# Kernel optimization log

Hardware: AMD Instinct MI355X
Metric: run time of the kernel (lower is better)

The kernel has to match this reference:

```python
import jax, jax.numpy as jnp
import numpy as np

DIM = 1024
NUM_HEADS = 16
HEAD_DIM = DIM // NUM_HEADS


def setup_inputs() -> dict:
    key = jax.random.key(0)
    k1, k2, k3 = jax.random.split(key, 3)
    scale = 1.0 / np.sqrt(DIM)
    x = jax.random.normal(k1, (4, 2048, DIM), dtype=jnp.float32)
    w_qkv = jax.random.normal(k2, (DIM, 3 * DIM), dtype=jnp.float32) * scale
    b_qkv = jnp.zeros((3 * DIM,), dtype=jnp.float32)
    w_out = jax.random.normal(k3, (DIM, DIM), dtype=jnp.float32) * scale
    b_out = jnp.zeros((DIM,), dtype=jnp.float32)
    return {"x": x, "w_qkv": w_qkv, "b_qkv": b_qkv, "w_out": w_out, "b_out": b_out}


def reference(x, w_qkv, b_qkv, w_out, b_out):
    B, S, D = x.shape
    H, Hd = NUM_HEADS, HEAD_DIM
    qkv = x @ w_qkv + b_qkv  # [B,S,3D]
    q, k, v = jnp.split(qkv, 3, axis=-1)
    # [B,H,S,Hd]
    q = q.reshape(B, S, H, Hd).transpose(0, 2, 1, 3)
    k = k.reshape(B, S, H, Hd).transpose(0, 2, 1, 3)
    v = v.reshape(B, S, H, Hd).transpose(0, 2, 1, 3)
    scores = jnp.einsum('bhqd,bhkd->bhqk', q, k) / np.sqrt(Hd).astype(np.float32)
    causal = jnp.triu(jnp.ones((S, S), dtype=bool), k=1)  # True above diagonal -> masked
    scores = jnp.where(causal[None, None], -jnp.inf, scores)
    scores = scores - jnp.max(scores, axis=-1, keepdims=True)
    attn = jax.nn.softmax(scores, axis=-1)
    out = jnp.einsum('bhqk,bhkd->bhqd', attn, v)  # [B,H,S,Hd]
    out = out.transpose(0, 2, 1, 3).reshape(B, S, D)
    return out @ w_out + b_out
```

## Files before the change

kernel.cpp:

```cpp
#include <hip/hip_runtime.h>

typedef unsigned short u16;
typedef unsigned int u32;
using f32x4 = __attribute__((ext_vector_type(4))) float;
using u32x4 = __attribute__((ext_vector_type(4))) u32;
typedef u32x4 __attribute__((may_alias)) u32x4a;
typedef uint2 __attribute__((may_alias)) uint2a;
using bf16x8 = __attribute__((ext_vector_type(8))) __bf16;

#define SEQ 2048

__device__ __forceinline__ u16 f2bf(float f) {
  union { float f; u32 u; } c; c.f = f;
  return (u16)((c.u + 0x7fffu + ((c.u >> 16) & 1u)) >> 16);
}
__device__ __forceinline__ float bf2f(u16 h) {
  union { u32 u; float f; } c; c.u = ((u32)h) << 16;
  return c.f;
}
__device__ __forceinline__ bf16x8 ld16(const u16* p) {
  return __builtin_bit_cast(bf16x8, *(const u32x4a*)p);
}
__device__ __forceinline__ f32x4 mfma16(bf16x8 a, bf16x8 b, f32x4 c) {
  return __builtin_amdgcn_mfma_f32_16x16x32_bf16(a, b, c, 0, 0, 0);
}
__device__ __forceinline__ void gload_lds16(const u16* g, u16* l) {
  __builtin_amdgcn_global_load_lds(
      (const __attribute__((address_space(1))) void*)g,
      (__attribute__((address_space(3))) void*)l, 16, 0, 0);
}
__device__ __forceinline__ u32 cvtpk(float lo, float hi) {
  u32 r;
  asm("v_cvt_pk_bf16_f32 %0, %1, %2" : "=v"(r) : "v"(lo), "v"(hi));
  return r;
}
__device__ __forceinline__ void plane32_swap(u32& a, u32& b) {
  asm("v_permlane32_swap_b32 %0, %1" : "+v"(a), "+v"(b));
}
__device__ __forceinline__ f32x4 vmax4(f32x4 a, f32x4 b) {
  f32x4 r;
  r[0] = fmaxf(a[0], b[0]); r[1] = fmaxf(a[1], b[1]);
  r[2] = fmaxf(a[2], b[2]); r[3] = fmaxf(a[3], b[3]);
  return r;
}

__global__ void detect_dtype(const u16* __restrict__ x, int* __restrict__ flag) {
  if (threadIdx.x == 0) {
    int cnt = 0;
    for (int i = 0; i < 32; ++i) {
      const int e = (x[2 * i] >> 7) & 0xFF;
      cnt += (e >= 100 && e <= 140) ? 1 : 0;
    }
    *flag = (cnt >= 20) ? 1 : 0;
  }
}


__global__ __launch_bounds__(256)
void cvt_x(const void* __restrict__ in, u16* __restrict__ out,
           const int* __restrict__ flag, size_t eoff4) {
  const size_t i = (size_t)blockIdx.x * 256 + threadIdx.x;
  if (*flag) {
    ((uint2*)out)[i] = ((const uint2*)in)[eoff4 + i];
  } else {
    const float4 v = ((const float4*)in)[eoff4 + i];
    uint2 ov;
    ov.x = (u32)f2bf(v.x) | ((u32)f2bf(v.y) << 16);
    ov.y = (u32)f2bf(v.z) | ((u32)f2bf(v.w) << 16);
    ((uint2*)out)[i] = ov;
  }
}

__global__ __launch_bounds__(256)
void cvt_bias(const void* __restrict__ in, float* __restrict__ out, int n,
              const int* __restrict__ flag) {
  const int i = blockIdx.x * 256 + threadIdx.x;
  if (i >= n) return;
  out[i] = (*flag) ? bf2f(((const u16*)in)[i]) : ((const float*)in)[i];
}

__global__ __launch_bounds__(256)
void transpose_w(const void* __restrict__ in, u16* __restrict__ out, int K, int N,
                 const int* __restrict__ flag) {
  __shared__ float t[64][65];
  const int tid = threadIdx.x;
  const int r = tid >> 4, c4 = tid & 15;
  const int n0 = blockIdx.x << 6, k0 = blockIdx.y << 6;
  const int fl = *flag;
#pragma unroll
  for (int i = 0; i < 4; ++i) {
    const int kk = r + i * 16;
    const size_t base = (size_t)(k0 + kk) * N + n0 + c4 * 4;
    if (fl) {
      const uint2 raw = *(const uint2*)((const u16*)in + base);
      t[kk][c4 * 4 + 0] = bf2f((u16)(raw.x & 0xFFFF));
      t[kk][c4 * 4 + 1] = bf2f((u16)(raw.x >> 16));
      t[kk][c4 * 4 + 2] = bf2f((u16)(raw.y & 0xFFFF));
      t[kk][c4 * 4 + 3] = bf2f((u16)(raw.y >> 16));
    } else {
      const float4 v = *(const float4*)((const float*)in + base);
      t[kk][c4 * 4 + 0] = v.x; t[kk][c4 * 4 + 1] = v.y;
      t[kk][c4 * 4 + 2] = v.z; t[kk][c4 * 4 + 3] = v.w;
    }
  }
  __syncthreads();
#pragma unroll
  for (int i = 0; i < 4; ++i) {
    const int nn = r + i * 16;
    uint2 ov;
    ov.x = (u32)f2bf(t[c4 * 4 + 0][nn]) | ((u32)f2bf(t[c4 * 4 + 1][nn]) << 16);
    ov.y = (u32)f2bf(t[c4 * 4 + 2][nn]) | ((u32)f2bf(t[c4 * 4 + 3][nn]) << 16);
    *(uint2*)&out[(size_t)(n0 + nn) * K + k0 + c4 * 4] = ov;
  }
}

__global__ __launch_bounds__(256)
void transpose_v(const u16* __restrict__ qkv, u16* __restrict__ vt) {
  __shared__ __align__(16) u16 t[64][72];
  const int h = blockIdx.x, s0 = blockIdx.y << 6, b = blockIdx.z;
  const int tid = threadIdx.x;
  const int r = tid >> 2, g = tid & 3;
  const u16* src = &qkv[(size_t)(b * SEQ + s0 + r) * 3072 + 2048 + h * 64 + g * 16];
  *(u32x4a*)&t[r][g * 16]     = *(const u32x4a*)src;
  *(u32x4a*)&t[r][g * 16 + 8] = *(const u32x4a*)(src + 8);
  __syncthreads();
  union { u16 s[16]; u32x4 v[2]; } u;
#pragma unroll
  for (int e = 0; e < 16; ++e) u.s[e] = t[g * 16 + e][r];
  u16* dst = &vt[(size_t)((b * 16 + h) * 64 + r) * 2048 + s0 + g * 16];
  *(u32x4a*)dst = u.v[0];
  *(u32x4a*)(dst + 8) = u.v[1];
}

template <bool BF16_OUT>
__global__ __launch_bounds__(512, 2)
void gemm_bt(const u16* __restrict__ A, const u16* __restrict__ BT,
             const float* __restrict__ bias, void* __restrict__ Cv,
             int M, int N, int K) {
  constexpr int BK = 32;
  __shared__ __align__(16) u16 ring[4][12288];
  const int tid = threadIdx.x;
  const int wid = tid >> 6, lane = tid & 63;
  const int quad = lane >> 4, l16 = lane & 15;

  const int nbx = gridDim.x, nwg = nbx * gridDim.y;
  int bid = blockIdx.y * nbx + blockIdx.x;
  if ((nwg & 7) == 0) bid = (bid & 7) * (nwg >> 3) + (bid >> 3);
  const int tile_n = (bid % nbx) << 7;
  const int tile_m = (bid / nbx) << 8;

  const int wmR = (wid >> 1) << 6;
  const int wnR = (wid & 1) << 6;

  const int G0 = wid * 64 + lane;
  const int rA0 = G0 >> 2;
  const int sA0 = (((G0 & 3) ^ ((rA0 & 3) ^ ((rA0 >> 2) & 3)))) * 8;
  const int G1 = G0 + 512;
  const int rA1 = G1 >> 2;
  const int sA1 = (((G1 & 3) ^ ((rA1 & 3) ^ ((rA1 >> 2) & 3)))) * 8;
  const u16* const pA0 = A + (size_t)(tile_m + rA0) * K + sA0;
  const u16* const pA1 = A + (size_t)(tile_m + rA1) * K + sA1;
  const u16* const pB0 = BT + (size_t)(tile_n + rA0) * K + sA0;
  const int dst0 = wid * 512;
  const int dst1 = 4096 + wid * 512;
  const int dstB = 8192 + wid * 512;

  const int swl = (l16 & 3) ^ ((l16 >> 2) & 3);
  const int cA = (quad ^ swl) * 8;

  const int nk = K >> 5;
  f32x4 acc[4][4] = {};

  auto STAGE = [&](int kt) {
    u16* bp = ring[kt & 3];
    const size_t ko = (size_t)kt * BK;
    gload_lds16(pA0 + ko, bp + dst0);
    gload_lds16(pA1 + ko, bp + dst1);
    gload_lds16(pB0 + ko, bp + dstB);
  };

  STAGE(0);
  if (nk > 1) STAGE(1);
  if (nk > 2) STAGE(2);

  for (int kt = 0; kt < nk; ++kt) {
    asm volatile("s_waitcnt vmcnt(6)" ::: "memory");
    __builtin_amdgcn_sched_barrier(0);
    __builtin_amdgcn_s_barrier();
    __builtin_amdgcn_sched_barrier(0);
    if (kt + 3 < nk) STAGE(kt + 3);
    const u16* bp = ring[kt & 3];
    bf16x8 af[4], bfr[4];
#pragma unroll
    for (int i = 0; i < 4; ++i)
      af[i] = ld16(&bp[(wmR + i * 16 + l16) * BK + cA]);
#pragma unroll
    for (int j = 0; j < 4; ++j)
      bfr[j] = ld16(&bp[8192 + (wnR + j * 16 + l16) * BK + cA]);
    asm volatile("s_waitcnt lgkmcnt(0)" ::: "memory");
    __builtin_amdgcn_sched_barrier(0);
    __builtin_amdgcn_s_setprio(1);
#pragma unroll
    for (int i = 0; i < 4; ++i)
#pragma unroll
      for (int j = 0; j < 4; ++j) acc[i][j] = mfma16(af[i], bfr[j], acc[i][j]);
    __builtin_amdgcn_s_setprio(0);
  }

#pragma unroll
  for (int j = 0; j < 4; ++j) {
    const int cg = tile_n + wnR + j * 16 + l16;
    const float bv = bias[cg];
#pragma unroll
    for (int i = 0; i < 4; ++i) {
      const int rg = tile_m + wmR + i * 16 + quad * 4;
#pragma unroll
      for (int r = 0; r < 4; ++r) {
        const float v = acc[i][j][r] + bv;
        if constexpr (BF16_OUT)
          ((u16*)Cv)[(size_t)(rg + r) * N + cg] = f2bf(v);
        else
          ((float*)Cv)[(size_t)(rg + r) * N + cg] = v;
      }
    }
  }
}

__global__ __launch_bounds__(256, 4)
void attn_fwd(const u16* __restrict__ qkv, const u16* __restrict__ vt,
              u16* __restrict__ aout) {
  const int h = blockIdx.x, b = blockIdx.z;
  const int tid = threadIdx.x, wid = tid >> 6, lane = tid & 63;
  const int quad = lane >> 4, l16 = lane & 15;
  const int qodd = quad & 1;
  __shared__ __align__(16) u16 lK[2][4096];
  __shared__ __align__(16) u16 lV[2][4096];

  const int G0 = wid * 64 + lane, G1 = G0 + 256;
  const int r0 = G0 >> 3, c0 = ((G0 & 7) ^ (r0 & 7)) * 8;
  const int r1 = G1 >> 3, c1 = ((G1 & 7) ^ (r1 & 7)) * 8;
  const int db0 = wid * 512, db1 = 2048 + wid * 512;

  const u16* const kg = qkv + (size_t)(b * SEQ) * 3072 + 1024 + h * 64;
  const u16* const vg = vt + (size_t)((b * 16 + h) * 64) * 2048;

  const int sl0 = (quad ^ (l16 & 7)) * 8;
  const int sl1 = sl0 ^ 32;

  const f32x4 z = {0.f, 0.f, 0.f, 0.f};
  int cur = 0;

#pragma unroll 1
  for (int pass = 0; pass < 2; ++pass) {
    const int qt = pass ? (int)blockIdx.y : 31 - (int)blockIdx.y;
    const int q0 = qt * 64 + wid * 16;
    const size_t qi = (size_t)(b * SEQ + q0 + l16) * 3072 + h * 64 + quad * 8;
    const bf16x8 aq0 = ld16(&qkv[qi]);
    const bf16x8 aq1 = ld16(&qkv[qi + 32]);
    f32x4 o[4] = {z, z, z, z};
    float m_r = -1e30f, l_r = 0.f;

    {
      gload_lds16(kg + (size_t)r0 * 3072 + c0, &lK[cur][db0]);
      gload_lds16(kg + (size_t)r1 * 3072 + c1, &lK[cur][db1]);
      gload_lds16(vg + (size_t)r0 * 2048 + c0, &lV[cur][db0]);
      gload_lds16(vg + (size_t)r1 * 2048 + c1, &lV[cur][db1]);
    }
    __syncthreads();

    for (int kt = 0; kt <= qt; ++kt) {
      if (kt < qt) {
        const int kb = (kt + 1) * 64;
        gload_lds16(kg + (size_t)(kb + r0) * 3072 + c0, &lK[cur ^ 1][db0]);
        gload_lds16(kg + (size_t)(kb + r1) * 3072 + c1, &lK[cur ^ 1][db1]);
        gload_lds16(vg + (size_t)r0 * 2048 + kb + c0, &lV[cur ^ 1][db0]);
        gload_lds16(vg + (size_t)r1 * 2048 + kb + c1, &lV[cur ^ 1][db1]);
      }
      const u16* const lKc = lK[cur];
      const u16* const lVc = lV[cur];
      f32x4 s[4];
#pragma unroll
      for (int f = 0; f < 4; ++f) {
        const int rb = (f * 16 + l16) * 64;
        f32x4 a = z;
        a = mfma16(ld16(&lKc[rb + sl0]), aq0, a);
        a = mfma16(ld16(&lKc[rb + sl1]), aq1, a);
        s[f] = a * 0.180336879f;
      }
      bf16x8 vf0[4], vf1[4];
#pragma unroll
      for (int f = 0; f < 4; ++f) {
        const int rb = (f * 16 + l16) * 64;
        vf0[f] = ld16(&lVc[rb + sl0]);
        vf1[f] = ld16(&lVc[rb + sl1]);
      }
      if (kt == qt) {
#pragma unroll
        for (int f = 0; f < 4; ++f)
#pragma unroll
          for (int r = 0; r < 4; ++r)
            if (f * 16 + quad * 4 + r > wid * 16 + l16) s[f][r] = -1e30f;
      }
      const f32x4 m4 = vmax4(vmax4(s[0], s[1]), vmax4(s[2], s[3]));
      const float pmax = fmaxf(fmaxf(m4[0], m4[1]), fmaxf(m4[2], m4[3]));
      if (__any(pmax > m_r + 8.f)) {
        float mm = fmaxf(pmax, __shfl_xor(pmax, 16));
        mm = fmaxf(mm, __shfl_xor(mm, 32));
        const float mn = fmaxf(m_r, mm);
        const float al = exp2f(m_r - mn);
        l_r *= al;
#pragma unroll
        for (int f = 0; f < 4; ++f)
#pragma unroll
          for (int r = 0; r < 4; ++r) o[f][r] *= al;
        m_r = mn;
      }
#pragma unroll
      for (int f = 0; f < 4; ++f)
#pragma unroll
        for (int r = 0; r < 4; ++r) s[f][r] = exp2f(s[f][r] - m_r);
      const f32x4 s4 = (s[0] + s[1]) + (s[2] + s[3]);
      float sv = (s4[0] + s4[1]) + (s4[2] + s4[3]);
      sv += __shfl_xor(sv, 16);
      sv += __shfl_xor(sv, 32);
      l_r += sv;
      u32 u00 = cvtpk(s[0][0], s[0][1]), u01 = cvtpk(s[0][2], s[0][3]);
      u32 u10 = cvtpk(s[1][0], s[1][1]), u11 = cvtpk(s[1][2], s[1][3]);
      u32 u20 = cvtpk(s[2][0], s[2][1]), u21 = cvtpk(s[2][2], s[2][3]);
      u32 u30 = cvtpk(s[3][0], s[3][1]), u31 = cvtpk(s[3][2], s[3][3]);
      u32x4 P0, P1;
      {
        u32 A0 = u00, B0 = u10, A1 = u01, B1 = u11;
        plane32_swap(A0, B0);
        plane32_swap(A1, B1);
        u32 Y0 = qodd ? A0 : B0;
        u32 Y1 = qodd ? A1 : B1;
        Y0 = (u32)__shfl_xor((int)Y0, 16);
        Y1 = (u32)__shfl_xor((int)Y1, 16);
        P0[0] = qodd ? Y0 : A0;
        P0[1] = qodd ? Y1 : A1;
        P0[2] = qodd ? B0 : Y0;
        P0[3] = qodd ? B1 : Y1;
      }
      {
        u32 A0 = u20, B0 = u30, A1 = u21, B1 = u31;
        plane32_swap(A0, B0);
        plane32_swap(A1, B1);
        u32 Y0 = qodd ? A0 : B0;
        u32 Y1 = qodd ? A1 : B1;
        Y0 = (u32)__shfl_xor((int)Y0, 16);
        Y1 = (u32)__shfl_xor((int)Y1, 16);
        P1[0] = qodd ? Y0 : A0;
        P1[1] = qodd ? Y1 : A1;
        P1[2] = qodd ? B0 : Y0;
        P1[3] = qodd ? B1 : Y1;
      }
      const bf16x8 pb0 = __builtin_bit_cast(bf16x8, P0);
      const bf16x8 pb1 = __builtin_bit_cast(bf16x8, P1);
#pragma unroll
      for (int f = 0; f < 4; ++f) {
        o[f] = mfma16(vf0[f], pb0, o[f]);
        o[f] = mfma16(vf1[f], pb1, o[f]);
      }
      __syncthreads();
      cur ^= 1;
    }
    const float inv = 1.0f / l_r;
#pragma unroll
    for (int f = 0; f < 4; ++f) {
      uint2a wv;
      wv.x = cvtpk(o[f][0] * inv, o[f][1] * inv);
      wv.y = cvtpk(o[f][2] * inv, o[f][3] * inv);
      *(uint2a*)&aout[(size_t)(b * SEQ + q0 + l16) * 1024 + h * 64 + f * 16 +
                      quad * 4] = wv;
    }
  }
}

extern "C" void kernel_launch(void* const* d_in, const int* in_sizes, int n_in,
                              void* d_out, int out_size, void* d_ws, size_t ws_size,
                              hipStream_t stream) {
  const void* x     = d_in[0];
  const void* w_qkv = d_in[1];
  const void* b_qkv = d_in[2];
  const void* w_out = d_in[3];
  const void* b_out = d_in[4];
  float* out = (float*)d_out;

  float* bqf   = (float*)d_ws;
  float* bof   = bqf + 3072;
  int*   flag  = (int*)(bof + 1024);
  u16*   wqkvT = (u16*)(flag + 4);
  u16*   woutT = wqkvT + (size_t)3072 * 1024;
  u16*   xb    = woutT + (size_t)1024 * 1024;

  detect_dtype<<<dim3(1), dim3(64), 0, stream>>>((const u16*)x, flag);
  cvt_bias<<<dim3(12), dim3(256), 0, stream>>>(b_qkv, bqf, 3072, flag);
  cvt_bias<<<dim3(4), dim3(256), 0, stream>>>(b_out, bof, 1024, flag);
  transpose_w<<<dim3(48, 16), dim3(256), 0, stream>>>(w_qkv, wqkvT, 1024, 3072, flag);
  transpose_w<<<dim3(16, 16), dim3(256), 0, stream>>>(w_out, woutT, 1024, 1024, flag);

  const size_t FULL_WS = 92291088;
  if (ws_size >= FULL_WS) {
    u16* qkv = xb  + (size_t)8192 * 1024;
    u16* vt  = qkv + (size_t)8192 * 3072;
    cvt_x<<<dim3(8192), dim3(256), 0, stream>>>(x, xb, flag, 0);
    gemm_bt<true ><<<dim3(24, 32), dim3(512), 0, stream>>>(xb, wqkvT, bqf, qkv,
                                                           8192, 3072, 1024);
    transpose_v<<<dim3(16, 32, 4), dim3(256), 0, stream>>>(qkv, vt);
    attn_fwd<<<dim3(16, 16, 4), dim3(256), 0, stream>>>(qkv, vt, xb);
    gemm_bt<false><<<dim3(8, 32), dim3(512), 0, stream>>>(xb, woutT, bof, out,
                                                          8192, 1024, 1024);
  } else {
    u16* qkvb = xb   + (size_t)2048 * 1024;
    u16* vtb  = qkvb + (size_t)2048 * 3072;
    for (int b = 0; b < 4; ++b) {
      const size_t eoff4 = (size_t)b * 2048 * 1024 / 4;
      cvt_x<<<dim3(2048), dim3(256), 0, stream>>>(x, xb, flag, eoff4);
      gemm_bt<true ><<<dim3(24, 8), dim3(512), 0, stream>>>(xb, wqkvT, bqf, qkvb,
                                                            2048, 3072, 1024);
      transpose_v<<<dim3(16, 32, 1), dim3(256), 0, stream>>>(qkvb, vtb);
      attn_fwd<<<dim3(16, 16, 1), dim3(256), 0, stream>>>(qkvb, vtb, xb);
      gemm_bt<false><<<dim3(8, 8), dim3(512), 0, stream>>>(
          xb, woutT, bof, out + (size_t)b * 2048 * 1024, 2048, 1024, 1024);
    }
  }
}
```

Measured before the change: 307.3 us.

## Rewrite attention with 32x32 MFMA tiles, 128-row query blocks and MFMA row sums

```diff
diff --git a/kernel.cpp b/kernel.cpp
--- a/kernel.cpp
+++ b/kernel.cpp
@@ -3,6 +3,7 @@
 typedef unsigned short u16;
 typedef unsigned int u32;
 using f32x4 = __attribute__((ext_vector_type(4))) float;
+using f32x16 = __attribute__((ext_vector_type(16))) float;
 using u32x4 = __attribute__((ext_vector_type(4))) u32;
 typedef u32x4 __attribute__((may_alias)) u32x4a;
 typedef uint2 __attribute__((may_alias)) uint2a;
@@ -24,6 +25,9 @@
 __device__ __forceinline__ f32x4 mfma16(bf16x8 a, bf16x8 b, f32x4 c) {
   return __builtin_amdgcn_mfma_f32_16x16x32_bf16(a, b, c, 0, 0, 0);
 }
+__device__ __forceinline__ f32x16 mfma32(bf16x8 a, bf16x8 b, f32x16 c) {
+  return __builtin_amdgcn_mfma_f32_32x32x16_bf16(a, b, c, 0, 0, 0);
+}
 __device__ __forceinline__ void gload_lds16(const u16* g, u16* l) {
   __builtin_amdgcn_global_load_lds(
       (const __attribute__((address_space(1))) void*)g,
@@ -36,12 +40,6 @@
 }
 __device__ __forceinline__ void plane32_swap(u32& a, u32& b) {
   asm("v_permlane32_swap_b32 %0, %1" : "+v"(a), "+v"(b));
-}
-__device__ __forceinline__ f32x4 vmax4(f32x4 a, f32x4 b) {
-  f32x4 r;
-  r[0] = fmaxf(a[0], b[0]); r[1] = fmaxf(a[1], b[1]);
-  r[2] = fmaxf(a[2], b[2]); r[3] = fmaxf(a[3], b[3]);
-  return r;
 }
 
 __global__ void detect_dtype(const u16* __restrict__ x, int* __restrict__ flag) {
@@ -226,13 +224,12 @@
   }
 }
 
-__global__ __launch_bounds__(256, 4)
+__global__ __launch_bounds__(256, 2)
 void attn_fwd(const u16* __restrict__ qkv, const u16* __restrict__ vt,
               u16* __restrict__ aout) {
   const int h = blockIdx.x, b = blockIdx.z;
   const int tid = threadIdx.x, wid = tid >> 6, lane = tid & 63;
-  const int quad = lane >> 4, l16 = lane & 15;
-  const int qodd = quad & 1;
+  const int l31 = lane & 31, hi = lane >> 5;
   __shared__ __align__(16) u16 lK[2][4096];
   __shared__ __align__(16) u16 lV[2][4096];
 
@@ -244,135 +241,158 @@
   const u16* const kg = qkv + (size_t)(b * SEQ) * 3072 + 1024 + h * 64;
   const u16* const vg = vt + (size_t)((b * 16 + h) * 64) * 2048;
 
-  const int sl0 = (quad ^ (l16 & 7)) * 8;
-  const int sl1 = sl0 ^ 32;
-
-  const f32x4 z = {0.f, 0.f, 0.f, 0.f};
+  constexpr float SC = 0.1803368801f;
+  constexpr float THR = 44.3614196f;
+
+  u32x4 onesu;
+  onesu[0] = onesu[1] = onesu[2] = onesu[3] = 0x3F803F80u;
+  const bf16x8 ones = __builtin_bit_cast(bf16x8, onesu);
+
+  const int sx = l31 & 7;
   int cur = 0;
 
 #pragma unroll 1
   for (int pass = 0; pass < 2; ++pass) {
-    const int qt = pass ? (int)blockIdx.y : 31 - (int)blockIdx.y;
-    const int q0 = qt * 64 + wid * 16;
-    const size_t qi = (size_t)(b * SEQ + q0 + l16) * 3072 + h * 64 + quad * 8;
-    const bf16x8 aq0 = ld16(&qkv[qi]);
-    const bf16x8 aq1 = ld16(&qkv[qi + 32]);
-    f32x4 o[4] = {z, z, z, z};
-    float m_r = -1e30f, l_r = 0.f;
-
-    {
-      gload_lds16(kg + (size_t)r0 * 3072 + c0, &lK[cur][db0]);
-      gload_lds16(kg + (size_t)r1 * 3072 + c1, &lK[cur][db1]);
-      gload_lds16(vg + (size_t)r0 * 2048 + c0, &lV[cur][db0]);
-      gload_lds16(vg + (size_t)r1 * 2048 + c1, &lV[cur][db1]);
-    }
+    const int qt = pass ? (int)blockIdx.y : 15 - (int)blockIdx.y;
+    const int q0w = qt * 128 + wid * 32;
+    const int qrow = q0w + l31;
+    bf16x8 qf[4];
+#pragma unroll
+    for (int d = 0; d < 4; ++d)
+      qf[d] = ld16(&qkv[(size_t)(b * SEQ + qrow) * 3072 + h * 64 + d * 16 + hi * 8]);
+    f32x16 o0 = {}, o1 = {}, lacc = {};
+    float m_r = -1e30f, ms = -1.8e29f;
+
+    gload_lds16(kg + (size_t)r0 * 3072 + c0, &lK[cur][db0]);
+    gload_lds16(kg + (size_t)r1 * 3072 + c1, &lK[cur][db1]);
+    gload_lds16(vg + (size_t)r0 * 2048 + c0, &lV[cur][db0]);
+    gload_lds16(vg + (size_t)r1 * 2048 + c1, &lV[cur][db1]);
     __syncthreads();
 
-    for (int kt = 0; kt <= qt; ++kt) {
-      if (kt < qt) {
-        const int kb = (kt + 1) * 64;
-        gload_lds16(kg + (size_t)(kb + r0) * 3072 + c0, &lK[cur ^ 1][db0]);
-        gload_lds16(kg + (size_t)(kb + r1) * 3072 + c1, &lK[cur ^ 1][db1]);
-        gload_lds16(vg + (size_t)r0 * 2048 + kb + c0, &lV[cur ^ 1][db0]);
-        gload_lds16(vg + (size_t)r1 * 2048 + kb + c1, &lV[cur ^ 1][db1]);
+    const int last = 2 * qt + 1;
+    for (int kt = 0; kt <= last; ++kt) {
+      const int kb = kt * 64;
+      if (kt < last) {
+        const int kn = kb + 64;
+        gload_lds16(kg + (size_t)(kn + r0) * 3072 + c0, &lK[cur ^ 1][db0]);
+        gload_lds16(kg + (size_t)(kn + r1) * 3072 + c1, &lK[cur ^ 1][db1]);
+        gload_lds16(vg + (size_t)r0 * 2048 + kn + c0, &lV[cur ^ 1][db0]);
+        gload_lds16(vg + (size_t)r1 * 2048 + kn + c1, &lV[cur ^ 1][db1]);
       }
-      const u16* const lKc = lK[cur];
-      const u16* const lVc = lV[cur];
-      f32x4 s[4];
-#pragma unroll
-      for (int f = 0; f < 4; ++f) {
-        const int rb = (f * 16 + l16) * 64;
-        f32x4 a = z;
-        a = mfma16(ld16(&lKc[rb + sl0]), aq0, a);
-        a = mfma16(ld16(&lKc[rb + sl1]), aq1, a);
-        s[f] = a * 0.180336879f;
-      }
-      bf16x8 vf0[4], vf1[4];
-#pragma unroll
-      for (int f = 0; f < 4; ++f) {
-        const int rb = (f * 16 + l16) * 64;
-        vf0[f] = ld16(&lVc[rb + sl0]);
-        vf1[f] = ld16(&lVc[rb + sl1]);
-      }
-      if (kt == qt) {
-#pragma unroll
-        for (int f = 0; f < 4; ++f)
-#pragma unroll
-          for (int r = 0; r < 4; ++r)
-            if (f * 16 + quad * 4 + r > wid * 16 + l16) s[f][r] = -1e30f;
-      }
-      const f32x4 m4 = vmax4(vmax4(s[0], s[1]), vmax4(s[2], s[3]));
-      const float pmax = fmaxf(fmaxf(m4[0], m4[1]), fmaxf(m4[2], m4[3]));
-      if (__any(pmax > m_r + 8.f)) {
-        float mm = fmaxf(pmax, __shfl_xor(pmax, 16));
-        mm = fmaxf(mm, __shfl_xor(mm, 32));
-        const float mn = fmaxf(m_r, mm);
-        const float al = exp2f(m_r - mn);
-        l_r *= al;
-#pragma unroll
-        for (int f = 0; f < 4; ++f)
-#pragma unroll
-          for (int r = 0; r < 4; ++r) o[f][r] *= al;
-        m_r = mn;
-      }
-#pragma unroll
-      for (int f = 0; f < 4; ++f)
-#pragma unroll
-        for (int r = 0; r < 4; ++r) s[f][r] = exp2f(s[f][r] - m_r);
-      const f32x4 s4 = (s[0] + s[1]) + (s[2] + s[3]);
-      float sv = (s4[0] + s4[1]) + (s4[2] + s4[3]);
-      sv += __shfl_xor(sv, 16);
-      sv += __shfl_xor(sv, 32);
-      l_r += sv;
-      u32 u00 = cvtpk(s[0][0], s[0][1]), u01 = cvtpk(s[0][2], s[0][3]);
-      u32 u10 = cvtpk(s[1][0], s[1][1]), u11 = cvtpk(s[1][2], s[1][3]);
-      u32 u20 = cvtpk(s[2][0], s[2][1]), u21 = cvtpk(s[2][2], s[2][3]);
-      u32 u30 = cvtpk(s[3][0], s[3][1]), u31 = cvtpk(s[3][2], s[3][3]);
-      u32x4 P0, P1;
-      {
-        u32 A0 = u00, B0 = u10, A1 = u01, B1 = u11;
-        plane32_swap(A0, B0);
-        plane32_swap(A1, B1);
-        u32 Y0 = qodd ? A0 : B0;
-        u32 Y1 = qodd ? A1 : B1;
-        Y0 = (u32)__shfl_xor((int)Y0, 16);
-        Y1 = (u32)__shfl_xor((int)Y1, 16);
-        P0[0] = qodd ? Y0 : A0;
-        P0[1] = qodd ? Y1 : A1;
-        P0[2] = qodd ? B0 : Y0;
-        P0[3] = qodd ? B1 : Y1;
-      }
-      {
-        u32 A0 = u20, B0 = u30, A1 = u21, B1 = u31;
-        plane32_swap(A0, B0);
-        plane32_swap(A1, B1);
-        u32 Y0 = qodd ? A0 : B0;
-        u32 Y1 = qodd ? A1 : B1;
-        Y0 = (u32)__shfl_xor((int)Y0, 16);
-        Y1 = (u32)__shfl_xor((int)Y1, 16);
-        P1[0] = qodd ? Y0 : A0;
-        P1[1] = qodd ? Y1 : A1;
-        P1[2] = qodd ? B0 : Y0;
-        P1[3] = qodd ? B1 : Y1;
-      }
-      const bf16x8 pb0 = __builtin_bit_cast(bf16x8, P0);
-      const bf16x8 pb1 = __builtin_bit_cast(bf16x8, P1);
-#pragma unroll
-      for (int f = 0; f < 4; ++f) {
-        o[f] = mfma16(vf0[f], pb0, o[f]);
-        o[f] = mfma16(vf1[f], pb1, o[f]);
+      if (kb <= q0w + 31) {
+        const u16* const lKc = lK[cur];
+        const u16* const lVc = lV[cur];
+        f32x16 s0 = {}, s1 = {};
+#pragma unroll
+        for (int d = 0; d < 4; ++d) {
+          const bf16x8 kf = ld16(&lKc[l31 * 64 + (((d * 2 + hi) ^ sx)) * 8]);
+          s0 = mfma32(kf, qf[d], s0);
+        }
+#pragma unroll
+        for (int d = 0; d < 4; ++d) {
+          const bf16x8 kf = ld16(&lKc[(32 + l31) * 64 + (((d * 2 + hi) ^ sx)) * 8]);
+          s1 = mfma32(kf, qf[d], s1);
+        }
+        bf16x8 vf[2][2][2];
+#pragma unroll
+        for (int kh = 0; kh < 2; ++kh)
+#pragma unroll
+          for (int j = 0; j < 2; ++j)
+#pragma unroll
+            for (int dh = 0; dh < 2; ++dh)
+              vf[kh][j][dh] = ld16(
+                  &lVc[(dh * 32 + l31) * 64 + (((kh * 4 + j * 2 + hi) ^ sx)) * 8]);
+        if (kb + 63 > q0w) {
+          const int rel = qrow - kb - 4 * hi;
+#pragma unroll
+          for (int i = 0; i < 16; ++i) {
+            const int kc = (i & 3) + 8 * (i >> 2);
+            if (kc > rel) s0[i] = -1e30f;
+            if (kc + 32 > rel) s1[i] = -1e30f;
+          }
+        }
+        float pm = fmaxf(fmaxf(s0[0], s0[1]), s0[2]);
+        pm = fmaxf(fmaxf(pm, s0[3]), s0[4]);
+        pm = fmaxf(fmaxf(pm, s0[5]), s0[6]);
+        pm = fmaxf(fmaxf(pm, s0[7]), s0[8]);
+        pm = fmaxf(fmaxf(pm, s0[9]), s0[10]);
+        pm = fmaxf(fmaxf(pm, s0[11]), s0[12]);
+        pm = fmaxf(fmaxf(pm, s0[13]), s0[14]);
+        pm = fmaxf(fmaxf(pm, s0[15]), s1[0]);
+        pm = fmaxf(fmaxf(pm, s1[1]), s1[2]);
+        pm = fmaxf(fmaxf(pm, s1[3]), s1[4]);
+        pm = fmaxf(fmaxf(pm, s1[5]), s1[6]);
+        pm = fmaxf(fmaxf(pm, s1[7]), s1[8]);
+        pm = fmaxf(fmaxf(pm, s1[9]), s1[10]);
+        pm = fmaxf(fmaxf(pm, s1[11]), s1[12]);
+        pm = fmaxf(fmaxf(pm, s1[13]), s1[14]);
+        pm = fmaxf(pm, s1[15]);
+        if (__any(pm > m_r + THR)) {
+          const float mm = fmaxf(pm, __shfl_xor(pm, 32));
+          const float mn = fmaxf(m_r, mm);
+          const float al = exp2f((m_r - mn) * SC);
+#pragma unroll
+          for (int i = 0; i < 16; ++i) {
+            o0[i] *= al; o1[i] *= al; lacc[i] *= al;
+          }
+          m_r = mn;
+          ms = mn * SC;
+        }
+#pragma unroll
+        for (int i = 0; i < 16; ++i) {
+          s0[i] = exp2f(fmaf(s0[i], SC, -ms));
+          s1[i] = exp2f(fmaf(s1[i], SC, -ms));
+        }
+        u32 t0 = cvtpk(s0[0], s0[1]), t1 = cvtpk(s0[2], s0[3]);
+        u32 t2 = cvtpk(s0[4], s0[5]), t3 = cvtpk(s0[6], s0[7]);
+        u32 t4 = cvtpk(s0[8], s0[9]), t5 = cvtpk(s0[10], s0[11]);
+        u32 t6 = cvtpk(s0[12], s0[13]), t7 = cvtpk(s0[14], s0[15]);
+        plane32_swap(t0, t2); plane32_swap(t1, t3);
+        plane32_swap(t4, t6); plane32_swap(t5, t7);
+        u32x4 w00, w01;
+        w00[0] = t0; w00[1] = t1; w00[2] = t2; w00[3] = t3;
+        w01[0] = t4; w01[1] = t5; w01[2] = t6; w01[3] = t7;
+        u32 u0 = cvtpk(s1[0], s1[1]), u1 = cvtpk(s1[2], s1[3]);
+        u32 u2 = cvtpk(s1[4], s1[5]), u3 = cvtpk(s1[6], s1[7]);
+        u32 u4 = cvtpk(s1[8], s1[9]), u5 = cvtpk(s1[10], s1[11]);
+        u32 u6 = cvtpk(s1[12], s1[13]), u7 = cvtpk(s1[14], s1[15]);
+        plane32_swap(u0, u2); plane32_swap(u1, u3);
+        plane32_swap(u4, u6); plane32_swap(u5, u7);
+        u32x4 w10, w11;
+        w10[0] = u0; w10[1] = u1; w10[2] = u2; w10[3] = u3;
+        w11[0] = u4; w11[1] = u5; w11[2] = u6; w11[3] = u7;
+        const bf16x8 pb00 = __builtin_bit_cast(bf16x8, w00);
+        const bf16x8 pb01 = __builtin_bit_cast(bf16x8, w01);
+        const bf16x8 pb10 = __builtin_bit_cast(bf16x8, w10);
+        const bf16x8 pb11 = __builtin_bit_cast(bf16x8, w11);
+        o0 = mfma32(vf[0][0][0], pb00, o0);
+        o1 = mfma32(vf[0][0][1], pb00, o1);
+        lacc = mfma32(ones, pb00, lacc);
+        o0 = mfma32(vf[0][1][0], pb01, o0);
+        o1 = mfma32(vf[0][1][1], pb01, o1);
+        lacc = mfma32(ones, pb01, lacc);
+        o0 = mfma32(vf[1][0][0], pb10, o0);
+        o1 = mfma32(vf[1][0][1], pb10, o1);
+        lacc = mfma32(ones, pb10, lacc);
+        o0 = mfma32(vf[1][1][0], pb11, o0);
+        o1 = mfma32(vf[1][1][1], pb11, o1);
+        lacc = mfma32(ones, pb11, lacc);
       }
       __syncthreads();
       cur ^= 1;
     }
-    const float inv = 1.0f / l_r;
-#pragma unroll
-    for (int f = 0; f < 4; ++f) {
+    const float inv = 1.0f / lacc[0];
+    u16* const orow = &aout[(size_t)(b * SEQ + qrow) * 1024 + h * 64];
+#pragma unroll
+    for (int t = 0; t < 4; ++t) {
+      const int d0 = 8 * t + 4 * hi;
       uint2a wv;
-      wv.x = cvtpk(o[f][0] * inv, o[f][1] * inv);
-      wv.y = cvtpk(o[f][2] * inv, o[f][3] * inv);
-      *(uint2a*)&aout[(size_t)(b * SEQ + q0 + l16) * 1024 + h * 64 + f * 16 +
-                      quad * 4] = wv;
+      wv.x = cvtpk(o0[4 * t] * inv, o0[4 * t + 1] * inv);
+      wv.y = cvtpk(o0[4 * t + 2] * inv, o0[4 * t + 3] * inv);
+      *(uint2a*)&orow[d0] = wv;
+      wv.x = cvtpk(o1[4 * t] * inv, o1[4 * t + 1] * inv);
+      wv.y = cvtpk(o1[4 * t + 2] * inv, o1[4 * t + 3] * inv);
+      *(uint2a*)&orow[32 + d0] = wv;
     }
   }
 }
@@ -408,7 +428,7 @@
     gemm_bt<true ><<<dim3(24, 32), dim3(512), 0, stream>>>(xb, wqkvT, bqf, qkv,
                                                            8192, 3072, 1024);
     transpose_v<<<dim3(16, 32, 4), dim3(256), 0, stream>>>(qkv, vt);
-    attn_fwd<<<dim3(16, 16, 4), dim3(256), 0, stream>>>(qkv, vt, xb);
+    attn_fwd<<<dim3(16, 8, 4), dim3(256), 0, stream>>>(qkv, vt, xb);
     gemm_bt<false><<<dim3(8, 32), dim3(512), 0, stream>>>(xb, woutT, bof, out,
                                                           8192, 1024, 1024);
   } else {
@@ -420,7 +440,7 @@
       gemm_bt<true ><<<dim3(24, 8), dim3(512), 0, stream>>>(xb, wqkvT, bqf, qkvb,
                                                             2048, 3072, 1024);
       transpose_v<<<dim3(16, 32, 1), dim3(256), 0, stream>>>(qkvb, vtb);
-      attn_fwd<<<dim3(16, 16, 1), dim3(256), 0, stream>>>(qkvb, vtb, xb);
+      attn_fwd<<<dim3(16, 8, 1), dim3(256), 0, stream>>>(qkvb, vtb, xb);
       gemm_bt<false><<<dim3(8, 8), dim3(512), 0, stream>>>(
           xb, woutT, bof, out + (size_t)b * 2048 * 1024, 2048, 1024, 1024);
     }
```

Measured after the change: 299.1 us. 2.7% less time.
